# Performance work log

Measured on AMD Instinct MI355X. Metric: run time of the kernel, lower is better.

The kernel has to match this reference:

```python
import jax, jax.numpy as jnp
import numpy as np

# --- static config (matches init_kwargs) ---
C = 384        # channels
H = 8          # num_heads
HD = C // H    # head_dim = 48
K = 1024       # patch_size (window)
BASE = 100.0   # rope_freq
MAX_POS = 4096
GRID_SIZE = 0.02
LN_EPS = 1e-5


def _interleave8(x, y, z):
    """Morton-interleave the low 8 bits of x,y,z -> 24-bit code (int32)."""
    key = jnp.zeros_like(x)
    for i in range(8):
        m = 1 << i
        key = key | ((x & m) << (2 * i + 2)) | ((y & m) << (2 * i + 1)) | ((z & m) << (2 * i))
    return key


def _serialize_points(xyz):
    """xyz: (B,3,N) -> (order (B,N) int32, grid (B,N,3) int32). Z-order sort."""
    pts = jnp.transpose(xyz, (0, 2, 1))                       # (B,N,3)
    grid = ((pts - pts.min(axis=1, keepdims=True)) / GRID_SIZE).astype(jnp.int32)
    grid = jnp.clip(grid, 0, 65535)
    gx, gy, gz = grid[..., 0], grid[..., 1], grid[..., 2]
    lo = _interleave8(gx & 255, gy & 255, gz & 255)           # low 24 bits of Morton code
    hi = _interleave8((gx >> 8) & 255, (gy >> 8) & 255, (gz >> 8) & 255)  # high word
    # 48-bit Morton order == lexsort with hi as primary key, lo secondary
    order = jax.vmap(lambda l, h: jnp.lexsort((l, h)))(lo, hi)
    return order.astype(jnp.int32), grid


def _rope_tables(d):
    inv_freq = 1.0 / (BASE ** (jnp.arange(0, d, 2, dtype=jnp.float32) / d))
    t = jnp.arange(MAX_POS, dtype=jnp.float32)
    freqs = t[:, None] * inv_freq[None, :]                    # (MAX_POS, d/2)
    freqs = jnp.concatenate([freqs, freqs], axis=-1)          # (MAX_POS, d)
    return jnp.cos(freqs), jnp.sin(freqs)


def _rotate_half(x):
    h = x.shape[-1] // 2
    return jnp.concatenate([-x[..., h:], x[..., :h]], axis=-1)


def _point_rope(tok, pos):
    """tok: (B,H,N,D) with D%3==0; pos: (B,N,3) int grid coords."""
    D = tok.shape[-1]
    d = D // 3
    pos = jnp.clip(pos, 0, MAX_POS - 1)
    cos, sin = _rope_tables(d)
    outs = []
    for axis, ch in enumerate(jnp.split(tok, 3, axis=-1)):
        p = pos[:, :, axis]                                   # (B,N)
        c = cos[p][:, None]                                   # (B,1,N,d)
        s = sin[p][:, None]
        outs.append(ch * c + _rotate_half(ch) * s)
    return jnp.concatenate(outs, axis=-1)


def _layernorm(x, g, b):
    mu = x.mean(axis=-1, keepdims=True)
    var = ((x - mu) ** 2).mean(axis=-1, keepdims=True)
    return (x - mu) * jax.lax.rsqrt(var + LN_EPS) * g + b


def _forward(x, xyz, ln1_g, ln1_b, qkv_w, qkv_b, proj_w, proj_b,
             ln2_g, ln2_b, ffn_w1, ffn_b1, ffn_w2, ffn_b2):
    B, C_, N = x.shape
    order, grid = _serialize_points(xyz)
    x_sorted = jnp.take_along_axis(x, order[:, None, :], axis=2)          # (B,C,N)
    grid_sorted = jnp.take_along_axis(grid, order[:, :, None], axis=1)    # (B,N,3)
    x_t = jnp.transpose(x_sorted, (0, 2, 1))                              # (B,N,C)
    shortcut = x_t
    xn = _layernorm(x_t, ln1_g, ln1_b)
    pad = (K - N % K) % K
    if pad > 0:
        xn = jnp.pad(xn, ((0, 0), (0, pad), (0, 0)))
        grid_sorted = jnp.pad(grid_sorted, ((0, 0), (0, pad), (0, 0)))
    Np = xn.shape[1]
    nw = Np // K
    qkv = (xn @ qkv_w + qkv_b).reshape(B, Np, 3, H, HD)
    q = jnp.transpose(qkv[:, :, 0], (0, 2, 1, 3))                         # (B,H,Np,HD)
    k = jnp.transpose(qkv[:, :, 1], (0, 2, 1, 3))
    v = jnp.transpose(qkv[:, :, 2], (0, 2, 1, 3))
    q = _point_rope(q, grid_sorted)
    k = _point_rope(k, grid_sorted)
    qw = q.reshape(B, H, nw, K, HD)
    kw = k.reshape(B, H, nw, K, HD)
    vw = v.reshape(B, H, nw, K, HD)
    scale = 1.0 / np.sqrt(HD).astype(np.float32)
    scores = jnp.einsum('bhwqd,bhwkd->bhwqk', qw, kw) * scale             # (B,H,nw,K,K)
    attn = jax.nn.softmax(scores, axis=-1)
    out = jnp.einsum('bhwqk,bhwkd->bhwqd', attn, vw)                      # (B,H,nw,K,HD)
    out = jnp.transpose(out, (0, 2, 3, 1, 4)).reshape(B, Np, C)
    out = out[:, :N]
    out = out @ proj_w + proj_b
    x_t = shortcut + out
    x_t = x_t + (jax.nn.gelu(_layernorm(x_t, ln2_g, ln2_b) @ ffn_w1 + ffn_b1,
                             approximate=False) @ ffn_w2 + ffn_b2)
    x_out = jnp.transpose(x_t, (0, 2, 1))                                 # (B,C,N)
    inv_order = jnp.argsort(order, axis=1)
    x_out = jnp.take_along_axis(x_out, inv_order[:, None, :], axis=2)
    return x_out


def setup_inputs() -> dict:
    key = jax.random.key(0)
    ks = jax.random.split(key, 12)
    B, N = 1, 16384
    s = 0.02
    return {
        'x': jax.random.normal(ks[0], (B, C, N), dtype=jnp.float32),
        'xyz': jax.random.uniform(ks[1], (B, 3, N), dtype=jnp.float32),
        'ln1_g': jnp.ones((C,), jnp.float32),
        'ln1_b': jnp.zeros((C,), jnp.float32),
        'qkv_w': jax.random.normal(ks[2], (C, 3 * C), jnp.float32) * s,
        'qkv_b': jnp.zeros((3 * C,), jnp.float32),
        'proj_w': jax.random.normal(ks[3], (C, C), jnp.float32) * s,
        'proj_b': jnp.zeros((C,), jnp.float32),
        'ln2_g': jnp.ones((C,), jnp.float32),
        'ln2_b': jnp.zeros((C,), jnp.float32),
        'ffn_w1': jax.random.normal(ks[4], (C, 4 * C), jnp.float32) * s,
        'ffn_b1': jnp.zeros((4 * C,), jnp.float32),
        'ffn_w2': jax.random.normal(ks[5], (4 * C, C), jnp.float32) * s,
        'ffn_b2': jnp.zeros((C,), jnp.float32),
    }


def reference(x, xyz, ln1_g, ln1_b, qkv_w, qkv_b, proj_w, proj_b,
              ln2_g, ln2_b, ffn_w1, ffn_b1, ffn_w2, ffn_b2):
    return _forward(x, xyz, ln1_g, ln1_b, qkv_w, qkv_b, proj_w, proj_b,
                    ln2_g, ln2_b, ffn_w1, ffn_b1, ffn_w2, ffn_b2)
```

## Files before the change

kernel.cpp:

```cpp
#include <hip/hip_runtime.h>
#include <hip/hip_bf16.h>

typedef unsigned short u16;
typedef unsigned int u32;
typedef unsigned long long u64;
typedef __attribute__((ext_vector_type(8))) short s16x8;
typedef __attribute__((ext_vector_type(4))) short s16x4;
typedef __attribute__((ext_vector_type(8))) unsigned short u16x8;
typedef __attribute__((ext_vector_type(4))) unsigned short u16x4;
typedef __attribute__((ext_vector_type(4))) float fx4;
typedef __attribute__((ext_vector_type(4))) unsigned int ux4;
typedef __attribute__((ext_vector_type(2))) unsigned int ux2;

__device__ __forceinline__ float bf2f(u16 u){ u32 x=((u32)u)<<16; return __builtin_bit_cast(float,x); }
__device__ __forceinline__ u16 f2bf(float f){ u32 x=__builtin_bit_cast(u32,f); return (u16)((x + 0x7FFFu + ((x>>16)&1u))>>16); }
__device__ __forceinline__ u32 cvtpk(float lo, float hi){
  u32 r; asm("v_cvt_pk_bf16_f32 %0, %1, %2" : "=v"(r) : "v"(lo), "v"(hi)); return r;
}

__device__ __forceinline__ s16x8 ld_bf8(const u16* p){
  s16x4 lo = *(const s16x4*)p;
  s16x4 hi = *(const s16x4*)(p+4);
  s16x8 r;
  r[0]=lo[0]; r[1]=lo[1]; r[2]=lo[2]; r[3]=lo[3];
  r[4]=hi[0]; r[5]=hi[1]; r[6]=hi[2]; r[7]=hi[3];
  return r;
}

__device__ __forceinline__ void gload16(const void* g, void* l){
  __builtin_amdgcn_global_load_lds((__attribute__((address_space(1))) void*)g,
                                   (__attribute__((address_space(3))) void*)l, 16, 0, 0);
}

__device__ __forceinline__ u64 spread3(u32 v){
  u64 x = v & 0xFFFFull;
  x = (x | (x<<32)) & 0x001f00000000ffffull;
  x = (x | (x<<16)) & 0x001f0000ff0000ffull;
  x = (x | (x<<8))  & 0x100f00f00f00f00full;
  x = (x | (x<<4))  & 0x10c30c30c30c30c3ull;
  x = (x | (x<<2))  & 0x1249249249249249ull;
  return x;
}

__global__ __launch_bounds__(256) void min3_kernel(const float* __restrict__ xyz, float* __restrict__ minsW, int N)
{
  __shared__ float red[3][4];
  int i = blockIdx.x*256 + threadIdx.x;
  int lane = threadIdx.x&63, wv = threadIdx.x>>6;
  float v0 = xyz[i], v1 = xyz[N+i], v2 = xyz[2*N+i];
  #pragma unroll
  for (int s=1;s<64;s<<=1){
    v0 = fminf(v0, __shfl_xor(v0,s));
    v1 = fminf(v1, __shfl_xor(v1,s));
    v2 = fminf(v2, __shfl_xor(v2,s));
  }
  if (lane==0){ red[0][wv]=v0; red[1][wv]=v1; red[2][wv]=v2; }
  __syncthreads();
  if (threadIdx.x < 3){
    float m = fminf(fminf(red[threadIdx.x][0],red[threadIdx.x][1]),
                    fminf(red[threadIdx.x][2],red[threadIdx.x][3]));
    minsW[blockIdx.x*3 + threadIdx.x] = m;
  }
}

__global__ __launch_bounds__(1024) void bsort_keys_kernel(const float* __restrict__ xyz, const float* __restrict__ minsW,
        u64* __restrict__ keys, int* __restrict__ gridO, int N)
{
  __shared__ u64 sk[2048];
  __shared__ float mnS[3];
  int t = threadIdx.x, bid = blockIdx.x;
  if (t < 192){
    float v = minsW[(t&63)*3 + (t>>6)];
    #pragma unroll
    for (int s=1;s<64;s<<=1) v = fminf(v, __shfl_xor(v,s));
    if ((t&63)==0) mnS[t>>6] = v;
  }
  __syncthreads();
  float mx0=mnS[0], mx1=mnS[1], mx2=mnS[2];
  int i0 = bid*2048;
  #pragma unroll
  for (int p=0;p<2;p++){
    int i = i0 + t + p*1024;
    int gx=(int)((xyz[i]-mx0)/0.02f);     gx = gx<0?0:(gx>65535?65535:gx);
    int gy=(int)((xyz[N+i]-mx1)/0.02f);   gy = gy<0?0:(gy>65535?65535:gy);
    int gz=(int)((xyz[2*N+i]-mx2)/0.02f); gz = gz<0?0:(gz>65535?65535:gz);
    gridO[i*3+0]=gx; gridO[i*3+1]=gy; gridO[i*3+2]=gz;
    u64 mort = (spread3((u32)gx)<<2)|(spread3((u32)gy)<<1)|spread3((u32)gz);
    sk[t + p*1024] = (mort<<14) | (u64)i;
  }
  for (int size=2; size<=2048; size<<=1){
    for (int stride=size>>1; stride>0; stride>>=1){
      __syncthreads();
      int i = 2*t - (t & (stride-1));
      int j = i + stride;
      u64 a = sk[i], b = sk[j];
      bool up = ((i & size) == 0);
      if ((a > b) == up){ sk[i]=b; sk[j]=a; }
    }
  }
  __syncthreads();
  keys[i0 + t] = sk[t];
  keys[i0 + 1024 + t] = sk[t+1024];
}

template<bool FINAL>
__global__ __launch_bounds__(256) void merge_kernel(const u64* __restrict__ src, u64* __restrict__ dst,
        int* __restrict__ order, int L, int N)
{
  int gt = blockIdx.x*256 + threadIdx.x;
  int d0 = gt*4;
  if (d0 >= N) return;
  int pair = d0 / (2*L);
  int base = pair*2*L;
  int ld = d0 - base;
  const u64* A = src + base;
  const u64* B = A + L;
  int lo = ld > L ? ld - L : 0;
  int hi = ld < L ? ld : L;
  while (lo < hi){
    int mid = (lo+hi)>>1;
    if (A[mid] <= B[ld-1-mid]) lo = mid+1; else hi = mid;
  }
  int i = lo, j = ld - lo;
  u64* out = dst + base + ld;
  int* oout = order + base + ld;
  u64 a = (i < L) ? A[i] : ~0ull;
  u64 b = (j < L) ? B[j] : ~0ull;
  #pragma unroll
  for (int e=0;e<4;e++){
    u64 v;
    if (a <= b){ v = a; i++; a = (i<L)?A[i]:~0ull; }
    else       { v = b; j++; b = (j<L)?B[j]:~0ull; }
    out[e] = v;
    if (FINAL) oout[e] = (int)(v & 16383ull);
  }
}

__global__ __launch_bounds__(256) void wtrans4_kernel(const float* __restrict__ qkv_w, const float* __restrict__ proj_w,
    const float* __restrict__ w1, const float* __restrict__ w2,
    u16* __restrict__ qkv_wT, u16* __restrict__ proj_wT, u16* __restrict__ w1T, u16* __restrict__ w2T)
{
  __shared__ float tl[32][33];
  int bid = blockIdx.x;
  const float* W; u16* Wt; int K, Nc, lb;
  if (bid < 432)      { W=qkv_w;  Wt=qkv_wT;  K=384;  Nc=1152; lb=bid; }
  else if (bid < 576) { W=proj_w; Wt=proj_wT; K=384;  Nc=384;  lb=bid-432; }
  else if (bid < 1152){ W=w1;     Wt=w1T;     K=384;  Nc=1536; lb=bid-576; }
  else                { W=w2;     Wt=w2T;     K=1536; Nc=384;  lb=bid-1152; }
  int nb = Nc/32;
  int n0 = (lb % nb)*32;
  int k0 = (lb / nb)*32;
  int t=threadIdx.x; int r=t>>5, c=t&31;
  #pragma unroll
  for (int p=0;p<4;p++) tl[p*8+r][c] = W[(size_t)(k0+p*8+r)*Nc + n0+c];
  __syncthreads();
  #pragma unroll
  for (int p=0;p<4;p++) Wt[(size_t)(n0+p*8+r)*K + k0+c] = f2bf(tl[c][p*8+r]);
}

template<bool BF16IN>
__global__ __launch_bounds__(256) void ln32_kernel(const void* __restrict__ xin, const float* __restrict__ g,
     const float* __restrict__ b, u16* __restrict__ xn, int N)
{
  extern __shared__ char dsm[];
  float* tile = (float*)dsm;
  int n0 = blockIdx.x*32;
  int t = threadIdx.x;
  int tok32 = t&31, cg2 = t>>5;
  #pragma unroll 8
  for (int p=0;p<48;p++){
    int cc = p*8 + cg2;
    float v;
    if (BF16IN) v = bf2f(((const u16*)xin)[(size_t)cc*N + n0 + tok32]);
    else        v = ((const float*)xin)[(size_t)cc*N + n0 + tok32];
    tile[tok32*388 + cc] = v;
  }
  __syncthreads();
  int tok = t>>3, part = t&7;
  const float* row = tile + tok*388 + part*48;
  float s=0.f;
  #pragma unroll
  for (int j=0;j<48;j++) s += row[j];
  s += __shfl_xor(s,1); s += __shfl_xor(s,2); s += __shfl_xor(s,4);
  float mu = s*(1.0f/384.0f);
  float vr=0.f;
  #pragma unroll
  for (int j=0;j<48;j++){ float d=row[j]-mu; vr += d*d; }
  vr += __shfl_xor(vr,1); vr += __shfl_xor(vr,2); vr += __shfl_xor(vr,4);
  float rs = rsqrtf(vr*(1.0f/384.0f) + 1e-5f);
  u16* dst = xn + (size_t)(n0+tok)*384 + part*48;
  #pragma unroll
  for (int q=0;q<6;q++){
    float v[8];
    #pragma unroll
    for (int j=0;j<8;j++){
      int c = part*48 + q*8 + j;
      v[j] = (row[q*8+j]-mu)*rs*g[c] + b[c];
    }
    ux4 o;
    o[0]=cvtpk(v[0],v[1]); o[1]=cvtpk(v[2],v[3]); o[2]=cvtpk(v[4],v[5]); o[3]=cvtpk(v[6],v[7]);
    *(ux4*)(dst + q*8) = o;
  }
}

__device__ __forceinline__ float gelu_f(float v){
  return 0.5f*v*(1.0f + erff(v*0.7071067811865475f));
}

template<int EPI>
__global__ __launch_bounds__(512) void gemm256_kernel(const u16* __restrict__ A, const u16* __restrict__ Bt,
    const float* __restrict__ bias, u16* __restrict__ outB, int M, int Nout, int K)
{
  __shared__ u16 Al[256*64];
  __shared__ u16 Bl[128*64];
  int nmt = M>>8;
  int m0 = (blockIdx.x % nmt)<<8;
  int n0 = (blockIdx.x / nmt)<<7;
  int t = threadIdx.x, lane=t&63, wv=t>>6, wr=wv>>1, wc=wv&1;
  int fr = lane&15, fg = lane>>4;
  fx4 acc[4][4];
  #pragma unroll
  for (int i=0;i<4;i++)
  #pragma unroll
  for (int j=0;j<4;j++) acc[i][j]=(fx4){0.f,0.f,0.f,0.f};
  int srowA = wv*32 + (lane>>3);
  int srowB = wv*16 + (lane>>3);
  int swz  = ((lane&7) ^ ((lane>>3)&7)) * 8;
  const u16* ApL = A  + (size_t)(m0+srowA)*K + swz;
  const u16* BpL = Bt + (size_t)(n0+srowB)*K + swz;
  u16* AlW = Al + wv*2048 + lane*8;
  u16* BlW = Bl + wv*1024 + lane*8;
  const u16* a_base = Al + (wr*64+fr)*64;
  const u16* b_base = Bl + (wc*64+fr)*64;
  int swr = fr & 7;
  for (int k0=0;k0<K;k0+=64){
    #pragma unroll
    for (int i=0;i<4;i++) gload16(ApL + k0 + (size_t)i*8*K, AlW + i*512);
    #pragma unroll
    for (int i=0;i<2;i++) gload16(BpL + k0 + (size_t)i*8*K, BlW + i*512);
    __syncthreads();
    #pragma unroll
    for (int ks=0;ks<2;ks++){
      int soff = (((ks*4+fg) ^ swr) << 3);
      s16x8 a[4], b[4];
      #pragma unroll
      for (int mi=0;mi<4;mi++) a[mi] = *(const s16x8*)(a_base + mi*1024 + soff);
      #pragma unroll
      for (int ni=0;ni<4;ni++) b[ni] = *(const s16x8*)(b_base + ni*1024 + soff);
      #pragma unroll
      for (int mi=0;mi<4;mi++)
      #pragma unroll
      for (int ni=0;ni<4;ni++)
        acc[mi][ni] = __builtin_amdgcn_mfma_f32_16x16x32_bf16(a[mi], b[ni], acc[mi][ni], 0,0,0);
    }
    __syncthreads();
  }
  #pragma unroll
  for (int mi=0;mi<4;mi++)
  #pragma unroll
  for (int ni=0;ni<4;ni++){
    int c = n0 + wc*64 + ni*16 + fr;
    float bi = bias[c];
    int mb = m0 + wr*64 + mi*16 + fg*4;
    #pragma unroll
    for (int j=0;j<4;j++){
      float vv = acc[mi][ni][j] + bi;
      if (EPI==1) vv = gelu_f(vv);
      outB[(size_t)(mb+j)*Nout + c] = f2bf(vv);
    }
  }
}

template<int EPI>
__global__ __launch_bounds__(256) void gemm128x2_kernel(const u16* __restrict__ A, const u16* __restrict__ Bt,
    const float* __restrict__ bias, u16* __restrict__ outB, float* __restrict__ outF,
    const float* __restrict__ resF, const u16* __restrict__ resB, int M, int Nout, int K)
{
  __shared__ u16 Al[2][128*64];
  __shared__ u16 Bl[2][128*64];
  int nmt = M>>7;
  int m0 = (blockIdx.x % nmt)<<7;
  int n0 = (blockIdx.x / nmt)<<7;
  int t = threadIdx.x, lane=t&63, wv=t>>6, wr=wv>>1, wc=wv&1;
  int fr = lane&15, fg = lane>>4;
  fx4 acc[4][4];
  #pragma unroll
  for (int i=0;i<4;i++)
  #pragma unroll
  for (int j=0;j<4;j++) acc[i][j]=(fx4){0.f,0.f,0.f,0.f};
  int srow = wv*32 + (lane>>3);
  int swz  = ((lane&7) ^ ((lane>>3)&7)) * 8;
  const u16* ApL = A  + (size_t)(m0+srow)*K + swz;
  const u16* BpL = Bt + (size_t)(n0+srow)*K + swz;
  int woff = wv*2048 + lane*8;
  int swr = fr & 7;
  for (int k0=0;k0<K;k0+=128){
    #pragma unroll
    for (int i=0;i<4;i++){
      gload16(ApL + k0 +      (size_t)i*8*K, Al[0] + woff + i*512);
      gload16(BpL + k0 +      (size_t)i*8*K, Bl[0] + woff + i*512);
      gload16(ApL + k0 + 64 + (size_t)i*8*K, Al[1] + woff + i*512);
      gload16(BpL + k0 + 64 + (size_t)i*8*K, Bl[1] + woff + i*512);
    }
    __syncthreads();
    #pragma unroll
    for (int sub=0;sub<2;sub++){
      const u16* a_base = Al[sub] + (wr*64+fr)*64;
      const u16* b_base = Bl[sub] + (wc*64+fr)*64;
      #pragma unroll
      for (int ks=0;ks<2;ks++){
        int soff = (((ks*4+fg) ^ swr) << 3);
        s16x8 a[4], b[4];
        #pragma unroll
        for (int mi=0;mi<4;mi++) a[mi] = *(const s16x8*)(a_base + mi*1024 + soff);
        #pragma unroll
        for (int ni=0;ni<4;ni++) b[ni] = *(const s16x8*)(b_base + ni*1024 + soff);
        #pragma unroll
        for (int mi=0;mi<4;mi++)
        #pragma unroll
        for (int ni=0;ni<4;ni++)
          acc[mi][ni] = __builtin_amdgcn_mfma_f32_16x16x32_bf16(a[mi], b[ni], acc[mi][ni], 0,0,0);
      }
    }
    __syncthreads();
  }
  if (EPI==2){
    #pragma unroll
    for (int mi=0;mi<4;mi++)
    #pragma unroll
    for (int ni=0;ni<4;ni++){
      int c = n0 + wc*64 + ni*16 + fr;
      float bi = bias[c];
      size_t idx = (size_t)c*M + m0 + wr*64 + mi*16 + fg*4;
      fx4 r4 = *(const fx4*)(resF + idx);
      ux2 p;
      p[0] = cvtpk(acc[mi][ni][0]+bi+r4[0], acc[mi][ni][1]+bi+r4[1]);
      p[1] = cvtpk(acc[mi][ni][2]+bi+r4[2], acc[mi][ni][3]+bi+r4[3]);
      *(ux2*)(outB + idx) = p;
    }
  } else {
    #pragma unroll
    for (int mi=0;mi<4;mi++)
    #pragma unroll
    for (int ni=0;ni<4;ni++){
      int c = n0 + wc*64 + ni*16 + fr;
      float bi = bias[c];
      size_t idx = (size_t)c*M + m0 + wr*64 + mi*16 + fg*4;
      ux2 rb = *(const ux2*)(resB + idx);
      fx4 o;
      o[0] = acc[mi][ni][0] + bi + bf2f((u16)rb[0]);
      o[1] = acc[mi][ni][1] + bi + bf2f((u16)(rb[0]>>16));
      o[2] = acc[mi][ni][2] + bi + bf2f((u16)rb[1]);
      o[3] = acc[mi][ni][3] + bi + bf2f((u16)(rb[1]>>16));
      *(fx4*)(outF + idx) = o;
    }
  }
}

#define LOG2_100_O8 0.8304820237218405f

__global__ __launch_bounds__(256) void rope_kernel(const u16* __restrict__ qkv, const int* __restrict__ order,
    const int* __restrict__ gridO, u16* __restrict__ Qp, u16* __restrict__ Kp, u16* __restrict__ Vp, int N)
{
  __shared__ float csm[64][24][2];
  __shared__ int origs[64];
  int i0 = blockIdx.x<<6;
  int t = threadIdx.x;
  if (t<64) origs[t] = order[i0+t];
  __syncthreads();
  for (int idx=t; idx<64*24; idx+=256){
    int tok = idx/24, slot = idx - tok*24;
    int a = slot>>3, fi = slot&7;
    int pos = gridO[(size_t)origs[tok]*3 + a];
    pos = pos<0?0:(pos>4095?4095:pos);
    float invf = __builtin_amdgcn_exp2f(-(float)fi * LOG2_100_O8);
    float ang = (float)pos * invf;
    csm[tok][slot][0] = __cosf(ang);
    csm[tok][slot][1] = __sinf(ang);
  }
  __syncthreads();
  int tok = t&63;
  int i = i0 + tok;
  const u16* src = qkv + (size_t)origs[tok]*1152;
  for (int h=t>>6; h<8; h+=4){
    size_t dst = ((size_t)h*N + i)*48;
    #pragma unroll
    for (int a=0;a<3;a++){
      u16x8 qa = *(const u16x8*)(src + h*48 + a*16);
      u16x8 qb = *(const u16x8*)(src + h*48 + a*16 + 8);
      u16x8 ka = *(const u16x8*)(src + 384 + h*48 + a*16);
      u16x8 kb = *(const u16x8*)(src + 384 + h*48 + a*16 + 8);
      float oqa[8], oqb[8], oka[8], okb[8];
      #pragma unroll
      for (int j=0;j<8;j++){
        float c0 = csm[tok][a*8+j][0], s0 = csm[tok][a*8+j][1];
        float ql = bf2f(qa[j]), qh = bf2f(qb[j]);
        float kl = bf2f(ka[j]), kh = bf2f(kb[j]);
        oqa[j] = ql*c0 - qh*s0;
        oqb[j] = qh*c0 + ql*s0;
        oka[j] = kl*c0 - kh*s0;
        okb[j] = kh*c0 + kl*s0;
      }
      ux4 OQa, OQb, OKa, OKb;
      #pragma unroll
      for (int p=0;p<4;p++){
        OQa[p]=cvtpk(oqa[2*p],oqa[2*p+1]);
        OQb[p]=cvtpk(oqb[2*p],oqb[2*p+1]);
        OKa[p]=cvtpk(oka[2*p],oka[2*p+1]);
        OKb[p]=cvtpk(okb[2*p],okb[2*p+1]);
      }
      *(ux4*)(Qp + dst + a*16) = OQa;
      *(ux4*)(Qp + dst + a*16 + 8) = OQb;
      *(ux4*)(Kp + dst + a*16) = OKa;
      *(ux4*)(Kp + dst + a*16 + 8) = OKb;
      u16x8 va = *(const u16x8*)(src + 768 + h*48 + a*16);
      u16x8 vb = *(const u16x8*)(src + 768 + h*48 + a*16 + 8);
      *(u16x8*)(Vp + dst + a*16) = va;
      *(u16x8*)(Vp + dst + a*16 + 8) = vb;
    }
  }
}

#define ATTN_SCALE 0.14433756729740643f
#define E2SCALE 0.2082354550504211f
#define DEFER_RAW 55.0f
#define KSTRIDE 68

__global__ __launch_bounds__(512) void attn7_kernel(const u16* __restrict__ Qp, const u16* __restrict__ Kp,
    const u16* __restrict__ Vp, const int* __restrict__ order, u16* __restrict__ attn, int N, int nw)
{
  __shared__ u16 Kl[2][64*KSTRIDE];
  __shared__ u16 Vl[2][48*KSTRIDE];
  __shared__ u16 Pl[8][32*KSTRIDE];
  int b = blockIdx.x;
  int hw = b & 127;
  int qc = b >> 7;
  int w = hw % nw, h = hw / nw;
  int t = threadIdx.x, lane = t&63, wv = t>>6;
  int fr = lane & 15, fg = lane >> 4;
  size_t base = ((size_t)h*N + (size_t)w*1024);
  int q0 = qc*256 + wv*32;
  bool kact = t < 384;
  int krow = t/6, kc = t - krow*6;
  const u16* ksrc = Kp + (base + krow)*48 + kc*8;
  int koff = krow*KSTRIDE + kc*8;
  int s2 = t - 128;
  bool vact = t >= 128;
  int vrow = s2/6, vc = s2 - vrow*6;
  const u16* vsrc = Vp + (base + vrow)*48 + vc*8;
  int vkey = vrow ^ (vc<<3);
  if (t < 256){
    ux2 z = {0,0};
    *(ux2*)&Kl[0][(t>>2)*KSTRIDE + 48 + (t&3)*4] = z;
    *(ux2*)&Kl[1][(t>>2)*KSTRIDE + 48 + (t&3)*4] = z;
  }
  s16x8 qf[2][2];
  s16x8 zf = {0,0,0,0,0,0,0,0};
  #pragma unroll
  for (int n=0;n<2;n++){
    const u16* qrow = Qp + (base + q0 + n*16 + fr)*48;
    qf[n][0] = ld_bf8(qrow + fg*8);
    qf[n][1] = (fg < 2) ? ld_bf8(qrow + 32 + fg*8) : zf;
  }
  s16x8 ones;
  #pragma unroll
  for (int j=0;j<8;j++) ones[j] = (short)0x3F80;

  float m0r = -3.4e38f, m1r = -3.4e38f;
  fx4 o00=(fx4){0.f,0.f,0.f,0.f}, o01=o00, o02=o00, o03=o00, o10=o00, o11=o00, o12=o00, o13=o00;
  u16* pl = Pl[wv];
  ux4 kreg = {0,0,0,0}, vreg = {0,0,0,0};
  if (kact) kreg = *(const ux4*)ksrc;
  if (vact) vreg = *(const ux4*)vsrc;
  if (kact){
    ux2 lo; lo[0]=kreg[0]; lo[1]=kreg[1];
    ux2 hi; hi[0]=kreg[2]; hi[1]=kreg[3];
    *(ux2*)(Kl[0]+koff) = lo; *(ux2*)(Kl[0]+koff+4) = hi;
  }
  if (vact){
    u16* vcp = Vl[0] + vkey;
    vcp[(vc*8+0)*KSTRIDE] = (u16)vreg[0];
    vcp[(vc*8+1)*KSTRIDE] = (u16)(vreg[0]>>16);
    vcp[(vc*8+2)*KSTRIDE] = (u16)vreg[1];
    vcp[(vc*8+3)*KSTRIDE] = (u16)(vreg[1]>>16);
    vcp[(vc*8+4)*KSTRIDE] = (u16)vreg[2];
    vcp[(vc*8+5)*KSTRIDE] = (u16)(vreg[2]>>16);
    vcp[(vc*8+6)*KSTRIDE] = (u16)vreg[3];
    vcp[(vc*8+7)*KSTRIDE] = (u16)(vreg[3]>>16);
  }
  __syncthreads();

  for (int c=0;c<16;c++){
    int cur = c & 1;
    const u16* kl = Kl[cur];
    const u16* vl = Vl[cur];
    if (c < 15){
      if (kact) kreg = *(const ux4*)(ksrc + (size_t)(c+1)*3072);
      if (vact) vreg = *(const ux4*)(vsrc + (size_t)(c+1)*3072);
    }
    fx4 s0[4], s1v[4];
    __builtin_amdgcn_s_setprio(1);
    #pragma unroll
    for (int m=0;m<4;m++){
      s0[m]=(fx4){0.f,0.f,0.f,0.f}; s1v[m]=s0[m];
      #pragma unroll
      for (int s=0;s<2;s++){
        s16x8 af = ld_bf8(kl + (m*16+fr)*KSTRIDE + s*32 + fg*8);
        s0[m]  = __builtin_amdgcn_mfma_f32_16x16x32_bf16(af, qf[0][s], s0[m],  0,0,0);
        s1v[m] = __builtin_amdgcn_mfma_f32_16x16x32_bf16(af, qf[1][s], s1v[m], 0,0,0);
      }
    }
    __builtin_amdgcn_s_setprio(0);
    float pm0 = -3.4e38f, pm1 = -3.4e38f;
    #pragma unroll
    for (int m=0;m<4;m++){
      float a0 = fmaxf(fmaxf(s0[m][0],s0[m][1]), fmaxf(s0[m][2],s0[m][3]));
      float a1 = fmaxf(fmaxf(s1v[m][0],s1v[m][1]), fmaxf(s1v[m][2],s1v[m][3]));
      pm0 = fmaxf(pm0, a0); pm1 = fmaxf(pm1, a1);
    }
    pm0 = fmaxf(pm0, __shfl_xor(pm0,16)); pm0 = fmaxf(pm0, __shfl_xor(pm0,32));
    pm1 = fmaxf(pm1, __shfl_xor(pm1,16)); pm1 = fmaxf(pm1, __shfl_xor(pm1,32));
    if (!__all((pm0 <= m0r + DEFER_RAW) & (pm1 <= m1r + DEFER_RAW))){
      float nm0 = fmaxf(m0r, pm0), nm1 = fmaxf(m1r, pm1);
      float f0 = __builtin_amdgcn_exp2f((m0r - nm0)*E2SCALE);
      float f1 = __builtin_amdgcn_exp2f((m1r - nm1)*E2SCALE);
      m0r = nm0; m1r = nm1;
      #pragma unroll
      for (int j=0;j<4;j++){
        float g0 = __shfl(f0, fg*4+j);
        float g1 = __shfl(f1, fg*4+j);
        o00[j]*=g0; o01[j]*=g0; o02[j]*=g0; o03[j]*=g0;
        o10[j]*=g1; o11[j]*=g1; o12[j]*=g1; o13[j]*=g1;
      }
    }
    #pragma unroll
    for (int m=0;m<4;m++){
      float e0[4], e1[4];
      #pragma unroll
      for (int j=0;j<4;j++){
        e0[j] = __builtin_amdgcn_exp2f((s0[m][j]-m0r)*E2SCALE);
        e1[j] = __builtin_amdgcn_exp2f((s1v[m][j]-m1r)*E2SCALE);
      }
      ux2 P0, P1;
      P0[0]=cvtpk(e0[0],e0[1]); P0[1]=cvtpk(e0[2],e0[3]);
      P1[0]=cvtpk(e1[0],e1[1]); P1[1]=cvtpk(e1[2],e1[3]);
      *(ux2*)&pl[(fr)*KSTRIDE + m*16 + fg*4]      = P0;
      *(ux2*)&pl[(16+fr)*KSTRIDE + m*16 + fg*4]   = P1;
    }
    __builtin_amdgcn_s_setprio(1);
    #pragma unroll
    for (int s=0;s<2;s++){
      int kb = s*32 + fg*8;
      s16x8 pa0 = ld_bf8(pl + fr*KSTRIDE + kb);
      s16x8 pa1 = ld_bf8(pl + (16+fr)*KSTRIDE + kb);
      s16x8 vb0 = ld_bf8(vl + (fr)*KSTRIDE    + (kb ^ ((fr)&56)));
      s16x8 vb1 = ld_bf8(vl + (16+fr)*KSTRIDE + (kb ^ ((16+fr)&56)));
      s16x8 vb2 = ld_bf8(vl + (32+fr)*KSTRIDE + (kb ^ ((32+fr)&56)));
      o00 = __builtin_amdgcn_mfma_f32_16x16x32_bf16(pa0, vb0, o00, 0,0,0);
      o01 = __builtin_amdgcn_mfma_f32_16x16x32_bf16(pa0, vb1, o01, 0,0,0);
      o02 = __builtin_amdgcn_mfma_f32_16x16x32_bf16(pa0, vb2, o02, 0,0,0);
      o03 = __builtin_amdgcn_mfma_f32_16x16x32_bf16(pa0, ones, o03, 0,0,0);
      o10 = __builtin_amdgcn_mfma_f32_16x16x32_bf16(pa1, vb0, o10, 0,0,0);
      o11 = __builtin_amdgcn_mfma_f32_16x16x32_bf16(pa1, vb1, o11, 0,0,0);
      o12 = __builtin_amdgcn_mfma_f32_16x16x32_bf16(pa1, vb2, o12, 0,0,0);
      o13 = __builtin_amdgcn_mfma_f32_16x16x32_bf16(pa1, ones, o13, 0,0,0);
    }
    __builtin_amdgcn_s_setprio(0);
    if (c < 15){
      u16* kln = Kl[cur^1];
      u16* vln = Vl[cur^1];
      if (kact){
        ux2 lo; lo[0]=kreg[0]; lo[1]=kreg[1];
        ux2 hi; hi[0]=kreg[2]; hi[1]=kreg[3];
        *(ux2*)(kln+koff) = lo; *(ux2*)(kln+koff+4) = hi;
      }
      if (vact){
        u16* vcp = vln + vkey;
        vcp[(vc*8+0)*KSTRIDE] = (u16)vreg[0];
        vcp[(vc*8+1)*KSTRIDE] = (u16)(vreg[0]>>16);
        vcp[(vc*8+2)*KSTRIDE] = (u16)vreg[1];
        vcp[(vc*8+3)*KSTRIDE] = (u16)(vreg[1]>>16);
        vcp[(vc*8+4)*KSTRIDE] = (u16)vreg[2];
        vcp[(vc*8+5)*KSTRIDE] = (u16)(vreg[2]>>16);
        vcp[(vc*8+6)*KSTRIDE] = (u16)vreg[3];
        vcp[(vc*8+7)*KSTRIDE] = (u16)(vreg[3]>>16);
      }
      __syncthreads();
    }
  }
  const int* ord = order + w*1024 + q0;
  #pragma unroll
  for (int j=0;j<4;j++){
    float inv0 = 1.0f / o03[j];
    float inv1 = 1.0f / o13[j];
    int orig0 = ord[fg*4+j];
    u16* dst0 = attn + (size_t)orig0*384 + h*48;
    dst0[fr]      = f2bf(o00[j]*inv0);
    dst0[16+fr]   = f2bf(o01[j]*inv0);
    dst0[32+fr]   = f2bf(o02[j]*inv0);
    int orig1 = ord[16 + fg*4+j];
    u16* dst1 = attn + (size_t)orig1*384 + h*48;
    dst1[fr]      = f2bf(o10[j]*inv1);
    dst1[16+fr]   = f2bf(o11[j]*inv1);
    dst1[32+fr]   = f2bf(o12[j]*inv1);
  }
}

extern "C" void kernel_launch(void* const* d_in, const int* in_sizes, int n_in,
                              void* d_out, int out_size, void* d_ws, size_t ws_size,
                              hipStream_t stream)
{
  (void)n_in; (void)out_size; (void)ws_size;
  const float* x     = (const float*)d_in[0];
  const float* xyz   = (const float*)d_in[1];
  const float* ln1_g = (const float*)d_in[2];
  const float* ln1_b = (const float*)d_in[3];
  const float* qkv_w = (const float*)d_in[4];
  const float* qkv_b = (const float*)d_in[5];
  const float* proj_w= (const float*)d_in[6];
  const float* proj_b= (const float*)d_in[7];
  const float* ln2_g = (const float*)d_in[8];
  const float* ln2_b = (const float*)d_in[9];
  const float* ffn_w1= (const float*)d_in[10];
  const float* ffn_b1= (const float*)d_in[11];
  const float* ffn_w2= (const float*)d_in[12];
  const float* ffn_b2= (const float*)d_in[13];
  int N = in_sizes[0]/384;
  int nw = N/1024;
  char* wsp = (char*)d_ws;
  size_t off = 0;
  auto alloc = [&](size_t bytes)->char*{ char* p = wsp + off; off = (off + bytes + 255) & ~(size_t)255; return p; };
  int*  order   = (int*)alloc((size_t)N*4);
  int*  gridO   = (int*)alloc((size_t)N*12);
  float* minsW  = (float*)alloc((size_t)(N/256)*12);
  u64*  keysA   = (u64*)alloc((size_t)N*8);
  u64*  keysB   = (u64*)alloc((size_t)N*8);
  u16*  qkv_wT  = (u16*)alloc((size_t)1152*384*2);
  u16*  proj_wT = (u16*)alloc((size_t)384*384*2);
  u16*  w1T     = (u16*)alloc((size_t)1536*384*2);
  u16*  w2T     = (u16*)alloc((size_t)384*1536*2);
  u16*  xn      = (u16*)alloc((size_t)N*384*2);
  u16*  Qp      = (u16*)alloc((size_t)N*48*8*2);
  u16*  Kp      = (u16*)alloc((size_t)N*48*8*2);
  u16*  Vp      = (u16*)alloc((size_t)N*48*8*2);
  u16*  qkvb    = (u16*)alloc((size_t)N*1152*2);
  u16*  y1b     = (u16*)alloc((size_t)N*384*2);
  u16*  attn    = xn;
  u16*  xn2     = qkvb;
  u16*  mid     = xn;
  float* outF = (float*)d_out;

  min3_kernel<<<N/256, 256, 0, stream>>>(xyz, minsW, N);
  bsort_keys_kernel<<<N/2048, 1024, 0, stream>>>(xyz, minsW, keysA, gridO, N);
  merge_kernel<false><<<N/1024, 256, 0, stream>>>(keysA, keysB, order, 2048, N);
  merge_kernel<false><<<N/1024, 256, 0, stream>>>(keysB, keysA, order, 4096, N);
  merge_kernel<true><<<N/1024, 256, 0, stream>>>(keysA, keysB, order, 8192, N);

  wtrans4_kernel<<<1728, 256, 0, stream>>>(qkv_w, proj_w, ffn_w1, ffn_w2, qkv_wT, proj_wT, w1T, w2T);
  ln32_kernel<false><<<N/32, 256, 32*388*4, stream>>>(x, ln1_g, ln1_b, xn, N);
  gemm256_kernel<0><<<(N/256)*(1152/128), 512, 0, stream>>>(xn, qkv_wT, qkv_b, qkvb, N, 1152, 384);
  rope_kernel<<<N/64, 256, 0, stream>>>(qkvb, order, gridO, Qp, Kp, Vp, N);
  attn7_kernel<<<8*nw*4, 512, 0, stream>>>(Qp, Kp, Vp, order, attn, N, nw);
  gemm128x2_kernel<2><<<(N/128)*(384/128), 256, 0, stream>>>(attn, proj_wT, proj_b, y1b, nullptr, x, nullptr, N, 384, 384);
  ln32_kernel<true><<<N/32, 256, 32*388*4, stream>>>(y1b, ln2_g, ln2_b, xn2, N);
  gemm256_kernel<1><<<(N/256)*(1536/128), 512, 0, stream>>>(xn2, w1T, ffn_b1, mid, N, 1536, 384);
  gemm128x2_kernel<3><<<(N/128)*(384/128), 256, 0, stream>>>(mid, w2T, ffn_b2, nullptr, outF, nullptr, y1b, N, 384, 1536);
}
```

Before: 265.1 us.

## Fuse RoPE and sorted-order scatter into QKV GEMM epilogue via inverse permutation

Removes the separate rope kernel and the intermediate qkv buffer. The QKV GEMM epilogue now adds bias, applies rotary embedding using lane shuffles to pair halves, and scatters results straight into the head-major Q/K/V layout. It uses an inverse sort permutation that the final merge pass now also writes. This saves a full write and read of the N×1152 intermediate, at the cost of scattered 2-byte stores and per-element sin/cos in the epilogue.

After: 245.4 us (median of 3 runs). -7.4%, faster.

```diff
diff --git a/kernel.cpp b/kernel.cpp
--- a/kernel.cpp
+++ b/kernel.cpp
@@ -105,7 +105,7 @@
 
 template<bool FINAL>
 __global__ __launch_bounds__(256) void merge_kernel(const u64* __restrict__ src, u64* __restrict__ dst,
-        int* __restrict__ order, int L, int N)
+        int* __restrict__ order, int* __restrict__ iorder, int L, int N)
 {
   int gt = blockIdx.x*256 + threadIdx.x;
   int d0 = gt*4;
@@ -132,7 +132,11 @@
     if (a <= b){ v = a; i++; a = (i<L)?A[i]:~0ull; }
     else       { v = b; j++; b = (j<L)?B[j]:~0ull; }
     out[e] = v;
-    if (FINAL) oout[e] = (int)(v & 16383ull);
+    if (FINAL){
+      int orig = (int)(v & 16383ull);
+      oout[e] = orig;
+      iorder[orig] = base + ld + e;
+    }
   }
 }
 
@@ -205,6 +209,93 @@
 
 __device__ __forceinline__ float gelu_f(float v){
   return 0.5f*v*(1.0f + erff(v*0.7071067811865475f));
+}
+
+#define LOG2_100_O8 0.8304820237218405f
+
+__global__ __launch_bounds__(512) void gemm256qkv_kernel(const u16* __restrict__ A, const u16* __restrict__ Bt,
+    const float* __restrict__ bias, const int* __restrict__ iorder, const int* __restrict__ gridO,
+    u16* __restrict__ Qp, u16* __restrict__ Kp, u16* __restrict__ Vp, int M, int K)
+{
+  __shared__ u16 Al[256*64];
+  __shared__ u16 Bl[128*64];
+  int nmt = M>>8;
+  int m0 = (blockIdx.x % nmt)<<8;
+  int n0 = (blockIdx.x / nmt)<<7;
+  int t = threadIdx.x, lane=t&63, wv=t>>6, wr=wv>>1, wc=wv&1;
+  int fr = lane&15, fg = lane>>4;
+  fx4 acc[4][4];
+  #pragma unroll
+  for (int i=0;i<4;i++)
+  #pragma unroll
+  for (int j=0;j<4;j++) acc[i][j]=(fx4){0.f,0.f,0.f,0.f};
+  int srowA = wv*32 + (lane>>3);
+  int srowB = wv*16 + (lane>>3);
+  int swz  = ((lane&7) ^ ((lane>>3)&7)) * 8;
+  const u16* ApL = A  + (size_t)(m0+srowA)*K + swz;
+  const u16* BpL = Bt + (size_t)(n0+srowB)*K + swz;
+  u16* AlW = Al + wv*2048 + lane*8;
+  u16* BlW = Bl + wv*1024 + lane*8;
+  const u16* a_base = Al + (wr*64+fr)*64;
+  const u16* b_base = Bl + (wc*64+fr)*64;
+  int swr = fr & 7;
+  for (int k0=0;k0<K;k0+=64){
+    #pragma unroll
+    for (int i=0;i<4;i++) gload16(ApL + k0 + (size_t)i*8*K, AlW + i*512);
+    #pragma unroll
+    for (int i=0;i<2;i++) gload16(BpL + k0 + (size_t)i*8*K, BlW + i*512);
+    __syncthreads();
+    #pragma unroll
+    for (int ks=0;ks<2;ks++){
+      int soff = (((ks*4+fg) ^ swr) << 3);
+      s16x8 a[4], b[4];
+      #pragma unroll
+      for (int mi=0;mi<4;mi++) a[mi] = *(const s16x8*)(a_base + mi*1024 + soff);
+      #pragma unroll
+      for (int ni=0;ni<4;ni++) b[ni] = *(const s16x8*)(b_base + ni*1024 + soff);
+      #pragma unroll
+      for (int mi=0;mi<4;mi++)
+      #pragma unroll
+      for (int ni=0;ni<4;ni++)
+        acc[mi][ni] = __builtin_amdgcn_mfma_f32_16x16x32_bf16(a[mi], b[ni], acc[mi][ni], 0,0,0);
+    }
+    __syncthreads();
+  }
+  float invf = __builtin_amdgcn_exp2f(-(float)(fr&7) * LOG2_100_O8);
+  bool hiLane = (fr & 8) != 0;
+  #pragma unroll
+  for (int mi=0;mi<4;mi++){
+    int tokb = m0 + wr*64 + mi*16 + fg*4;
+    int io4[4];
+    #pragma unroll
+    for (int j=0;j<4;j++) io4[j] = iorder[tokb+j];
+    #pragma unroll
+    for (int ni=0;ni<4;ni++){
+      int c = n0 + wc*64 + ni*16 + fr;
+      float bi = bias[c];
+      int sec = c/384;
+      int rem = c - sec*384;
+      int h = rem/48;
+      int a = (rem%48)>>4;
+      u16* dst = (sec==0) ? Qp : ((sec==1) ? Kp : Vp);
+      #pragma unroll
+      for (int j=0;j<4;j++){
+        float v = acc[mi][ni][j] + bi;
+        float outv;
+        if (sec < 2){
+          int pos = gridO[(tokb+j)*3 + a];
+          pos = pos>4095?4095:pos;
+          float ang = (float)pos * invf;
+          float cs = __cosf(ang), sn = __sinf(ang);
+          float p = __shfl_xor(v, 8);
+          outv = hiLane ? (v*cs + p*sn) : (v*cs - p*sn);
+        } else {
+          outv = v;
+        }
+        dst[((size_t)h*M + io4[j])*48 + a*16 + fr] = f2bf(outv);
+      }
+    }
+  }
 }
 
 template<int EPI>
@@ -353,70 +444,6 @@
       o[2] = acc[mi][ni][2] + bi + bf2f((u16)rb[1]);
       o[3] = acc[mi][ni][3] + bi + bf2f((u16)(rb[1]>>16));
       *(fx4*)(outF + idx) = o;
-    }
-  }
-}
-
-#define LOG2_100_O8 0.8304820237218405f
-
-__global__ __launch_bounds__(256) void rope_kernel(const u16* __restrict__ qkv, const int* __restrict__ order,
-    const int* __restrict__ gridO, u16* __restrict__ Qp, u16* __restrict__ Kp, u16* __restrict__ Vp, int N)
-{
-  __shared__ float csm[64][24][2];
-  __shared__ int origs[64];
-  int i0 = blockIdx.x<<6;
-  int t = threadIdx.x;
-  if (t<64) origs[t] = order[i0+t];
-  __syncthreads();
-  for (int idx=t; idx<64*24; idx+=256){
-    int tok = idx/24, slot = idx - tok*24;
-    int a = slot>>3, fi = slot&7;
-    int pos = gridO[(size_t)origs[tok]*3 + a];
-    pos = pos<0?0:(pos>4095?4095:pos);
-    float invf = __builtin_amdgcn_exp2f(-(float)fi * LOG2_100_O8);
-    float ang = (float)pos * invf;
-    csm[tok][slot][0] = __cosf(ang);
-    csm[tok][slot][1] = __sinf(ang);
-  }
-  __syncthreads();
-  int tok = t&63;
-  int i = i0 + tok;
-  const u16* src = qkv + (size_t)origs[tok]*1152;
-  for (int h=t>>6; h<8; h+=4){
-    size_t dst = ((size_t)h*N + i)*48;
-    #pragma unroll
-    for (int a=0;a<3;a++){
-      u16x8 qa = *(const u16x8*)(src + h*48 + a*16);
-      u16x8 qb = *(const u16x8*)(src + h*48 + a*16 + 8);
-      u16x8 ka = *(const u16x8*)(src + 384 + h*48 + a*16);
-      u16x8 kb = *(const u16x8*)(src + 384 + h*48 + a*16 + 8);
-      float oqa[8], oqb[8], oka[8], okb[8];
-      #pragma unroll
-      for (int j=0;j<8;j++){
-        float c0 = csm[tok][a*8+j][0], s0 = csm[tok][a*8+j][1];
-        float ql = bf2f(qa[j]), qh = bf2f(qb[j]);
-        float kl = bf2f(ka[j]), kh = bf2f(kb[j]);
-        oqa[j] = ql*c0 - qh*s0;
-        oqb[j] = qh*c0 + ql*s0;
-        oka[j] = kl*c0 - kh*s0;
-        okb[j] = kh*c0 + kl*s0;
-      }
-      ux4 OQa, OQb, OKa, OKb;
-      #pragma unroll
-      for (int p=0;p<4;p++){
-        OQa[p]=cvtpk(oqa[2*p],oqa[2*p+1]);
-        OQb[p]=cvtpk(oqb[2*p],oqb[2*p+1]);
-        OKa[p]=cvtpk(oka[2*p],oka[2*p+1]);
-        OKb[p]=cvtpk(okb[2*p],okb[2*p+1]);
-      }
-      *(ux4*)(Qp + dst + a*16) = OQa;
-      *(ux4*)(Qp + dst + a*16 + 8) = OQb;
-      *(ux4*)(Kp + dst + a*16) = OKa;
-      *(ux4*)(Kp + dst + a*16 + 8) = OKb;
-      u16x8 va = *(const u16x8*)(src + 768 + h*48 + a*16);
-      u16x8 vb = *(const u16x8*)(src + 768 + h*48 + a*16 + 8);
-      *(u16x8*)(Vp + dst + a*16) = va;
-      *(u16x8*)(Vp + dst + a*16 + 8) = vb;
     }
   }
 }
@@ -631,6 +658,7 @@
   size_t off = 0;
   auto alloc = [&](size_t bytes)->char*{ char* p = wsp + off; off = (off + bytes + 255) & ~(size_t)255; return p; };
   int*  order   = (int*)alloc((size_t)N*4);
+  int*  iorder  = (int*)alloc((size_t)N*4);
   int*  gridO   = (int*)alloc((size_t)N*12);
   float* minsW  = (float*)alloc((size_t)(N/256)*12);
   u64*  keysA   = (u64*)alloc((size_t)N*8);
@@ -643,23 +671,21 @@
   u16*  Qp      = (u16*)alloc((size_t)N*48*8*2);
   u16*  Kp      = (u16*)alloc((size_t)N*48*8*2);
   u16*  Vp      = (u16*)alloc((size_t)N*48*8*2);
-  u16*  qkvb    = (u16*)alloc((size_t)N*1152*2);
+  u16*  xn2     = (u16*)alloc((size_t)N*384*2);
   u16*  y1b     = (u16*)alloc((size_t)N*384*2);
   u16*  attn    = xn;
-  u16*  xn2     = qkvb;
   u16*  mid     = xn;
   float* outF = (float*)d_out;
 
   min3_kernel<<<N/256, 256, 0, stream>>>(xyz, minsW, N);
   bsort_keys_kernel<<<N/2048, 1024, 0, stream>>>(xyz, minsW, keysA, gridO, N);
-  merge_kernel<false><<<N/1024, 256, 0, stream>>>(keysA, keysB, order, 2048, N);
-  merge_kernel<false><<<N/1024, 256, 0, stream>>>(keysB, keysA, order, 4096, N);
-  merge_kernel<true><<<N/1024, 256, 0, stream>>>(keysA, keysB, order, 8192, N);
+  merge_kernel<false><<<N/1024, 256, 0, stream>>>(keysA, keysB, order, iorder, 2048, N);
+  merge_kernel<false><<<N/1024, 256, 0, stream>>>(keysB, keysA, order, iorder, 4096, N);
+  merge_kernel<true><<<N/1024, 256, 0, stream>>>(keysA, keysB, order, iorder, 8192, N);
 
   wtrans4_kernel<<<1728, 256, 0, stream>>>(qkv_w, proj_w, ffn_w1, ffn_w2, qkv_wT, proj_wT, w1T, w2T);
   ln32_kernel<false><<<N/32, 256, 32*388*4, stream>>>(x, ln1_g, ln1_b, xn, N);
-  gemm256_kernel<0><<<(N/256)*(1152/128), 512, 0, stream>>>(xn, qkv_wT, qkv_b, qkvb, N, 1152, 384);
-  rope_kernel<<<N/64, 256, 0, stream>>>(qkvb, order, gridO, Qp, Kp, Vp, N);
+  gemm256qkv_kernel<<<(N/256)*(1152/128), 512, 0, stream>>>(xn, qkv_wT, qkv_b, iorder, gridO, Qp, Kp, Vp, N, 384);
   attn7_kernel<<<8*nw*4, 512, 0, stream>>>(Qp, Kp, Vp, order, attn, N, nw);
   gemm128x2_kernel<2><<<(N/128)*(384/128), 256, 0, stream>>>(attn, proj_wT, proj_b, y1b, nullptr, x, nullptr, N, 384, 384);
   ln32_kernel<true><<<N/32, 256, 32*388*4, stream>>>(y1b, ln2_g, ln2_b, xn2, N);
```
